# Performance work log

Hardware: AMD Instinct MI355X
Metric: run time of the kernel (lower is better)

Reference implementation:

```python
import jax, jax.numpy as jnp
import numpy as np

N, E, G = 40000, 640000, 64
D_IN, D_EMB, D_HID, D_OUT = 128, 128, 128, 36


def setup_inputs() -> dict:
    key = jax.random.key(0)
    ks = jax.random.split(key, 12)
    x = jax.random.normal(ks[0], (N, D_IN), dtype=jnp.float32)
    edge_weight = jax.random.uniform(ks[1], (E,), dtype=jnp.float32)
    rho = jax.random.uniform(ks[2], (G,), dtype=jnp.float32)
    edge_index = jax.random.randint(ks[3], (2, E), 0, N, dtype=jnp.int32)
    batch = jnp.sort(jax.random.randint(ks[4], (N,), 0, G, dtype=jnp.int32))
    def lin(k, fi, fo):
        s = 1.0 / np.sqrt(fi)
        return jax.random.normal(k, (fi, fo), dtype=jnp.float32) * s
    conv_w = lin(ks[5], D_IN, D_EMB)
    conv_b = jnp.zeros((D_EMB,), jnp.float32)
    w1 = lin(ks[6], 2 * D_EMB + 1, D_HID); b1 = jnp.zeros((D_HID,), jnp.float32)
    w2 = lin(ks[7], D_HID, D_HID);        b2 = jnp.zeros((D_HID,), jnp.float32)
    w3 = lin(ks[8], D_HID, D_OUT);        b3 = jnp.zeros((D_OUT,), jnp.float32)
    return dict(x=x, edge_weight=edge_weight, rho=rho, conv_w=conv_w, conv_b=conv_b,
                w1=w1, b1=b1, w2=w2, b2=b2, w3=w3, b3=b3,
                edge_index=edge_index, batch=batch)


def _gcn_conv(h, edge_index, ew, W, b):
    # PyG GCNConv: add self-loops (weight 1), symmetric deg^-1/2 normalization,
    # linear transform, gather-scale-scatter aggregation, bias.
    n = h.shape[0]
    loop = jnp.arange(n, dtype=edge_index.dtype)
    src = jnp.concatenate([edge_index[0], loop])
    dst = jnp.concatenate([edge_index[1], loop])
    w_all = jnp.concatenate([ew, jnp.ones((n,), ew.dtype)])
    deg = jax.ops.segment_sum(w_all, dst, num_segments=n)
    dinv = jnp.where(deg > 0, jax.lax.rsqrt(deg), 0.0)
    norm = dinv[src] * w_all * dinv[dst]          # [E+N]
    hW = h @ W                                    # [N, D_EMB]
    msg = hW[src] * norm[:, None]                 # [E+N, D_EMB]
    return jax.ops.segment_sum(msg, dst, num_segments=n) + b


def reference(x, edge_weight, rho, conv_w, conv_b, w1, b1, w2, b2, w3, b3,
              edge_index, batch):
    h = jax.nn.relu(_gcn_conv(x, edge_index, edge_weight, conv_w, conv_b))
    g = G
    cnt = jax.ops.segment_sum(jnp.ones((h.shape[0],), h.dtype), batch, num_segments=g)
    hmax = jax.ops.segment_max(h, batch, num_segments=g)
    hmax = jnp.where(cnt[:, None] > 0, hmax, 0.0)
    hsum = jax.ops.segment_sum(h, batch, num_segments=g)
    hmean = hsum / jnp.maximum(cnt, 1.0)[:, None]
    hg = jnp.concatenate([hmax, hmean, rho[:, None]], axis=1)  # [G, 2*D_EMB+1]
    z = jax.nn.relu(hg @ w1 + b1)
    z = jax.nn.relu(z @ w2 + b2)
    return z @ w3 + b3
```

## Files before the change

### kernel.cpp

```cpp
#include <hip/hip_runtime.h>
#include <hip/hip_fp16.h>

static __device__ __forceinline__ float relu_f(float v) { return v > 0.f ? v : 0.f; }

typedef _Float16 half8 __attribute__((ext_vector_type(8)));
typedef float floatx4 __attribute__((ext_vector_type(4)));

#define ELL 96

static __device__ __forceinline__ float entry_w(unsigned int pk) {
  return __half2float(__ushort_as_half((unsigned short)(pk >> 16)));
}


__global__ __launch_bounds__(256) void count_fill_kernel(
    const int* __restrict__ src, const int* __restrict__ dst,
    const float* __restrict__ ew, unsigned long long* __restrict__ cnt,
    unsigned int* __restrict__ epack, int E,
    const float* __restrict__ W, _Float16* __restrict__ wt,
    const float* __restrict__ w1, float* __restrict__ w1t,
    const float* __restrict__ w2, float* __restrict__ w2t,
    const float* __restrict__ w3, float* __restrict__ w3t) {
  int i = blockIdx.x * blockDim.x + threadIdx.x;
  if (i < 16384) {
    int k = i >> 7, c = i & 127;
    wt[c * 128 + k] = (_Float16)W[i];
  } else if (i < 16384 + 32896) {
    int j = i - 16384;
    int k = j >> 7, c = j & 127;
    w1t[c * 260 + k] = w1[j];
  } else if (i < 16384 + 32896 + 16384) {
    int j = i - (16384 + 32896);
    int k = j >> 7, c = j & 127;
    w2t[c * 128 + k] = w2[j];
  } else if (i < 16384 + 32896 + 16384 + 4608) {
    int j = i - (16384 + 32896 + 16384);
    int k = j / 36, c = j - k * 36;
    w3t[c * 128 + k] = w3[j];
  }
  int e0 = i * 4;
  if (e0 >= E) return;
  if (e0 + 3 < E) {
    int4   s4 = *(const int4*)(src + e0);
    int4   d4 = *(const int4*)(dst + e0);
    float4 w4 = *(const float4*)(ew + e0);
    int   ss[4] = {s4.x, s4.y, s4.z, s4.w};
    int   dd[4] = {d4.x, d4.y, d4.z, d4.w};
    float ww[4] = {w4.x, w4.y, w4.z, w4.w};
    #pragma unroll
    for (int u = 0; u < 4; ++u) {
      unsigned long long pk = (1ull << 32) |
          (unsigned long long)__float2uint_rn(ww[u] * 16777216.f);
      unsigned long long old = atomicAdd(&cnt[dd[u]], pk);
      unsigned int r = (unsigned int)(old >> 32);
      if (r < ELL) {
        unsigned short w16 = __half_as_ushort(__float2half_rn(ww[u]));
        epack[(size_t)dd[u] * ELL + r] = (unsigned int)ss[u] | ((unsigned int)w16 << 16);
      }
    }
  } else {
    for (int e = e0; e < E; ++e) {
      float w = ew[e];
      unsigned long long pk = (1ull << 32) |
          (unsigned long long)__float2uint_rn(w * 16777216.f);
      unsigned long long old = atomicAdd(&cnt[dst[e]], pk);
      unsigned int r = (unsigned int)(old >> 32);
      if (r < ELL) {
        unsigned short w16 = __half_as_ushort(__float2half_rn(w));
        epack[(size_t)dst[e] * ELL + r] = (unsigned int)src[e] | ((unsigned int)w16 << 16);
      }
    }
  }
}


__global__ void premul_cast_kernel(const float4* __restrict__ x4,
                                   const unsigned long long* __restrict__ cnt,
                                   half8* __restrict__ xh8, int n) {
  int j = blockIdx.x * blockDim.x + threadIdx.x;
  if (j >= n * 16) return;
  int node = j >> 4;
  unsigned long long cv = cnt[node];
  float deg = 1.f + (float)(unsigned int)cv * (1.f / 16777216.f);
  float dinv = rsqrtf(deg);
  float4 a = x4[2 * j], b = x4[2 * j + 1];
  half8 o;
  o[0] = (_Float16)(a.x * dinv); o[1] = (_Float16)(a.y * dinv);
  o[2] = (_Float16)(a.z * dinv); o[3] = (_Float16)(a.w * dinv);
  o[4] = (_Float16)(b.x * dinv); o[5] = (_Float16)(b.y * dinv);
  o[6] = (_Float16)(b.z * dinv); o[7] = (_Float16)(b.w * dinv);
  xh8[j] = o;
}


__global__ __launch_bounds__(256) void agg_gemm_pool_kernel(const half8* __restrict__ xh8,
    const unsigned long long* __restrict__ cnt,
    const unsigned int* __restrict__ epack, const _Float16* __restrict__ wt,
    const float* __restrict__ bias, const int* __restrict__ batch,
    float* __restrict__ gmax, float* __restrict__ gsum, float* __restrict__ gcnt, int n) {
  __shared__ float sH[64 * 129];
  _Float16* sAgg = (_Float16*)sH;
  __shared__ int sBatch[64];
  int tid = threadIdx.x;
  int w = tid >> 6, lane = tid & 63;
  int grp = lane >> 4, sub = lane & 15;
  int quad = lane >> 4, c15 = lane & 15;
  int row0 = blockIdx.x * 64;
  int nb = n - row0; if (nb > 64) nb = 64;

  #pragma unroll
  for (int it = 0; it < 4; ++it) {
    int rloc = w * 16 + it * 4 + grp;
    int node = row0 + rloc;
    if (node >= n) node = n - 1;
    unsigned long long cv = cnt[node];
    int deg = (int)(unsigned int)(cv >> 32);
    if (deg > ELL) deg = ELL;
    float dn = rsqrtf(1.f + (float)(unsigned int)cv * (1.f / 16777216.f));
    half8 xv = xh8[(size_t)node * 16 + sub];
    float acc[8];
    #pragma unroll
    for (int c = 0; c < 8; ++c) acc[c] = dn * (float)xv[c];
    size_t base = (size_t)node * ELL;
    int dlen = (deg + 7) & ~7;
    uint4 pa, pb;
    if (dlen > 0) {
      pa = *(const uint4*)&epack[base];
      pb = *(const uint4*)&epack[base + 4];
    }
    for (int j = 0; j < dlen; j += 8) {
      size_t nxt = (j + 8 < dlen) ? base + j + 8 : base;
      uint4 na = *(const uint4*)&epack[nxt];
      uint4 nb2 = *(const uint4*)&epack[nxt + 4];
      unsigned int pk[8] = {pa.x, pa.y, pa.z, pa.w, pb.x, pb.y, pb.z, pb.w};
      half8 hx[8];
      #pragma unroll
      for (int u = 0; u < 8; ++u) {
        int sidx = (j + u < deg) ? (int)(pk[u] & 0xFFFFu) : node;
        hx[u] = xh8[(size_t)sidx * 16 + sub];
      }
      #pragma unroll
      for (int u = 0; u < 8; ++u) {
        float wgt = (j + u < deg) ? entry_w(pk[u]) * dn : 0.f;
        #pragma unroll
        for (int c = 0; c < 8; ++c) acc[c] += wgt * (float)hx[u][c];
      }
      pa = na; pb = nb2;
    }
    half8 outv;
    #pragma unroll
    for (int c = 0; c < 8; ++c) outv[c] = (_Float16)acc[c];
    *(half8*)&sAgg[rloc * 136 + sub * 8] = outv;
  }
  __syncthreads();

  half8 af[4];
  #pragma unroll
  for (int ks = 0; ks < 4; ++ks)
    af[ks] = *(const half8*)&sAgg[(w * 16 + c15) * 136 + ks * 32 + quad * 8];
  if (tid < nb) sBatch[tid] = batch[row0 + tid];
  __syncthreads();

  float bb[8];
  #pragma unroll
  for (int j = 0; j < 8; ++j) bb[j] = bias[j * 16 + c15];

  floatx4 acc[8] = {};
  #pragma unroll
  for (int ks = 0; ks < 4; ++ks) {
    #pragma unroll
    for (int j = 0; j < 8; ++j) {
      const half8* bptr =
          (const half8*)(wt + (size_t)(j * 16 + c15) * 128 + ks * 32 + quad * 8);
      acc[j] = __builtin_amdgcn_mfma_f32_16x16x32_f16(af[ks], *bptr, acc[j], 0, 0, 0);
    }
  }

  #pragma unroll
  for (int j = 0; j < 8; ++j) {
    int col = j * 16 + c15;
    #pragma unroll
    for (int r = 0; r < 4; ++r) {
      int row = w * 16 + quad * 4 + r;
      if (row < nb) sH[row * 129 + col] = relu_f(acc[j][r] + bb[j]);
    }
  }
  __syncthreads();

  if (tid < 128) {
    int c = tid;
    int cur = sBatch[0];
    float mx = 0.f, sm = 0.f;
    int cnt_ = 0;
    for (int r = 0; r < nb; ++r) {
      int g = sBatch[r];
      if (g != cur) {
        atomicMax((int*)&gmax[cur * 128 + c], __float_as_int(mx));
        atomicAdd(&gsum[cur * 128 + c], sm);
        if (c == 0) atomicAdd(&gcnt[cur], (float)cnt_);
        mx = 0.f; sm = 0.f; cnt_ = 0; cur = g;
      }
      float v = sH[r * 129 + c];
      mx = fmaxf(mx, v);
      sm += v;
      ++cnt_;
    }
    atomicMax((int*)&gmax[cur * 128 + c], __float_as_int(mx));
    atomicAdd(&gsum[cur * 128 + c], sm);
    if (c == 0) atomicAdd(&gcnt[cur], (float)cnt_);
  }
}


__global__ __launch_bounds__(256) void mlp_kernel(const float* __restrict__ gmax,
    const float* __restrict__ gsum, const float* __restrict__ gcnt,
    const float* __restrict__ rho,
    const float* __restrict__ w1t, const float* __restrict__ b1,
    const float* __restrict__ w2t, const float* __restrict__ b2,
    const float* __restrict__ w3t, const float* __restrict__ b3,
    float* __restrict__ out) {
  __shared__ float s_in[260];
  __shared__ float s_part[256];
  __shared__ float s_z1[128];
  __shared__ float s_z2[128];
  int g = blockIdx.x, t = threadIdx.x;
  int col = t & 127, seg = t >> 7;
  float inv_cnt = 1.f / fmaxf(gcnt[g], 1.f);
  if (t < 128) s_in[t] = gmax[g * 128 + t];
  else         s_in[t] = gsum[g * 128 + col] * inv_cnt;
  if (t == 0)  s_in[256] = rho[g];
  __syncthreads();

  float s;
  {
    const float4* wp = (const float4*)(w1t + (size_t)col * 260 + seg * 128);
    const float4* sp = (const float4*)(s_in + seg * 128);
    float a = 0.f, b = 0.f;
    #pragma unroll
    for (int q = 0; q < 32; q += 2) {
      float4 u0 = wp[q],     i0 = sp[q];
      float4 u1 = wp[q + 1], i1 = sp[q + 1];
      a += u0.x * i0.x + u0.y * i0.y + u0.z * i0.z + u0.w * i0.w;
      b += u1.x * i1.x + u1.y * i1.y + u1.z * i1.z + u1.w * i1.w;
    }
    s = a + b;
    s += seg ? s_in[256] * w1t[(size_t)col * 260 + 256] : b1[col];
  }
  s_part[t] = s;
  __syncthreads();
  if (t < 128) s_z1[t] = relu_f(s_part[t] + s_part[t + 128]);
  __syncthreads();

  {
    const float4* wp = (const float4*)(w2t + (size_t)col * 128 + seg * 64);
    const float4* sp = (const float4*)(s_z1 + seg * 64);
    float a = 0.f, b = 0.f;
    #pragma unroll
    for (int q = 0; q < 16; q += 2) {
      float4 u0 = wp[q],     i0 = sp[q];
      float4 u1 = wp[q + 1], i1 = sp[q + 1];
      a += u0.x * i0.x + u0.y * i0.y + u0.z * i0.z + u0.w * i0.w;
      b += u1.x * i1.x + u1.y * i1.y + u1.z * i1.z + u1.w * i1.w;
    }
    s = a + b + (seg ? 0.f : b2[col]);
  }
  s_part[t] = s;
  __syncthreads();
  if (t < 128) s_z2[t] = relu_f(s_part[t] + s_part[t + 128]);
  __syncthreads();

  if (t < 144) {
    int oc = t % 36, sg = t / 36;
    const float4* wp = (const float4*)(w3t + (size_t)oc * 128 + sg * 32);
    const float4* sp = (const float4*)(s_z2 + sg * 32);
    float a = 0.f;
    #pragma unroll
    for (int q = 0; q < 8; ++q) {
      float4 u = wp[q], iv = sp[q];
      a += u.x * iv.x + u.y * iv.y + u.z * iv.z + u.w * iv.w;
    }
    s_part[t] = a;
  }
  __syncthreads();
  if (t < 36)
    out[g * 36 + t] = b3[t] + s_part[t] + s_part[t + 36] + s_part[t + 72] + s_part[t + 108];
}


extern "C" void kernel_launch(void* const* d_in, const int* in_sizes, int n_in,
                              void* d_out, int out_size, void* d_ws, size_t ws_size,
                              hipStream_t stream) {
  const float* x      = (const float*)d_in[0];
  const float* ew     = (const float*)d_in[1];
  const float* rho    = (const float*)d_in[2];
  const float* conv_w = (const float*)d_in[3];
  const float* conv_b = (const float*)d_in[4];
  const float* w1 = (const float*)d_in[5];
  const float* b1 = (const float*)d_in[6];
  const float* w2 = (const float*)d_in[7];
  const float* b2 = (const float*)d_in[8];
  const float* w3 = (const float*)d_in[9];
  const float* b3 = (const float*)d_in[10];
  const int* eidx  = (const int*)d_in[11];
  const int* batch = (const int*)d_in[12];

  const int N = in_sizes[0] / 128;
  const int E = in_sizes[1];
  const int G = in_sizes[2];
  const int* srcp = eidx;
  const int* dstp = eidx + E;

  char* p = (char*)d_ws;
  auto carve = [&](size_t bytes) { char* r = p; p += (bytes + 255) & ~(size_t)255; return (void*)r; };
  char* zbase = p;
  unsigned long long* cnt  = (unsigned long long*)carve((size_t)N * 8);
  float*              gmax = (float*)             carve((size_t)G * 128 * 4);
  float*              gsum = (float*)             carve((size_t)G * 128 * 4);
  float*              gcnt = (float*)             carve((size_t)G * 4);
  size_t zbytes = (size_t)(p - zbase);
  unsigned int* epack = (unsigned int*)carve((size_t)N * ELL * 4);
  half8*        xh    = (half8*)       carve((size_t)N * 128 * 2);
  _Float16*     wt    = (_Float16*)    carve((size_t)128 * 128 * 2);
  float*        w1t   = (float*)       carve((size_t)128 * 260 * 4);
  float*        w2t   = (float*)       carve((size_t)128 * 128 * 4);
  float*        w3t   = (float*)       carve((size_t)36 * 128 * 4);

  hipMemsetAsync(zbase, 0, zbytes, stream);

  int nthr_cf = (E + 3) / 4;
  if (nthr_cf < 70272) nthr_cf = 70272;
  count_fill_kernel<<<(nthr_cf + 255) / 256, 256, 0, stream>>>(srcp, dstp, ew, cnt,
                                                               epack, E, conv_w, wt,
                                                               w1, w1t, w2, w2t, w3, w3t);
  premul_cast_kernel<<<(N * 16 + 255) / 256, 256, 0, stream>>>((const float4*)x, cnt, xh, N);
  agg_gemm_pool_kernel<<<(N + 63) / 64, 256, 0, stream>>>(xh, cnt, epack, wt, conv_b,
                                                          batch, gmax, gsum, gcnt, N);
  mlp_kernel<<<G, 256, 0, stream>>>(gmax, gsum, gcnt, rho, w1t, b1, w2t, b2, w3t, b3,
                                    (float*)d_out);
}
```

Before: 173.2 us.

## Split fused aggregation+GEMM+pool kernel into separate aggregation and GEMM-pool kernels

The neighbour-gather aggregation moves out of the LDS-heavy fused kernel into its own kernel. It uses no shared memory, handles one node per 16-thread group, and writes fp16 aggregated features to a new global buffer. The GEMM/pooling kernel now reads its MFMA A-fragments straight from that buffer instead of from LDS, which drops a barrier. The aim is higher occupancy and better latency hiding for the memory-bound gather loop. The cost is an extra launch and an extra write and read of an N×128 fp16 intermediate.

```diff
diff --git a/kernel.cpp b/kernel.cpp
--- a/kernel.cpp
+++ b/kernel.cpp
@@ -93,73 +93,74 @@
 }
 
 
-__global__ __launch_bounds__(256) void agg_gemm_pool_kernel(const half8* __restrict__ xh8,
+__global__ __launch_bounds__(256) void agg_kernel(const half8* __restrict__ xh8,
     const unsigned long long* __restrict__ cnt,
-    const unsigned int* __restrict__ epack, const _Float16* __restrict__ wt,
-    const float* __restrict__ bias, const int* __restrict__ batch,
+    const unsigned int* __restrict__ epack,
+    half8* __restrict__ hagg, int n) {
+  int tid = threadIdx.x;
+  int node = blockIdx.x * 16 + (tid >> 4);
+  int sub = tid & 15;
+  if (node >= n) return;
+  unsigned long long cv = cnt[node];
+  int deg = (int)(unsigned int)(cv >> 32);
+  if (deg > ELL) deg = ELL;
+  float dn = rsqrtf(1.f + (float)(unsigned int)cv * (1.f / 16777216.f));
+  half8 xv = xh8[(size_t)node * 16 + sub];
+  float acc[8];
+  #pragma unroll
+  for (int c = 0; c < 8; ++c) acc[c] = dn * (float)xv[c];
+  size_t base = (size_t)node * ELL;
+  int dlen = (deg + 7) & ~7;
+  uint4 pa, pb;
+  if (dlen > 0) {
+    pa = *(const uint4*)&epack[base];
+    pb = *(const uint4*)&epack[base + 4];
+  }
+  for (int j = 0; j < dlen; j += 8) {
+    size_t nxt = (j + 8 < dlen) ? base + j + 8 : base;
+    uint4 na = *(const uint4*)&epack[nxt];
+    uint4 nb2 = *(const uint4*)&epack[nxt + 4];
+    unsigned int pk[8] = {pa.x, pa.y, pa.z, pa.w, pb.x, pb.y, pb.z, pb.w};
+    half8 hx[8];
+    #pragma unroll
+    for (int u = 0; u < 8; ++u) {
+      int sidx = (j + u < deg) ? (int)(pk[u] & 0xFFFFu) : node;
+      hx[u] = xh8[(size_t)sidx * 16 + sub];
+    }
+    #pragma unroll
+    for (int u = 0; u < 8; ++u) {
+      float wgt = (j + u < deg) ? entry_w(pk[u]) * dn : 0.f;
+      #pragma unroll
+      for (int c = 0; c < 8; ++c) acc[c] += wgt * (float)hx[u][c];
+    }
+    pa = na; pb = nb2;
+  }
+  half8 outv;
+  #pragma unroll
+  for (int c = 0; c < 8; ++c) outv[c] = (_Float16)acc[c];
+  hagg[(size_t)node * 16 + sub] = outv;
+}
+
+
+__global__ __launch_bounds__(256) void gemm_pool_kernel(const half8* __restrict__ hagg,
+    const _Float16* __restrict__ wt, const float* __restrict__ bias,
+    const int* __restrict__ batch,
     float* __restrict__ gmax, float* __restrict__ gsum, float* __restrict__ gcnt, int n) {
   __shared__ float sH[64 * 129];
-  _Float16* sAgg = (_Float16*)sH;
   __shared__ int sBatch[64];
   int tid = threadIdx.x;
   int w = tid >> 6, lane = tid & 63;
-  int grp = lane >> 4, sub = lane & 15;
   int quad = lane >> 4, c15 = lane & 15;
   int row0 = blockIdx.x * 64;
   int nb = n - row0; if (nb > 64) nb = 64;
 
-  #pragma unroll
-  for (int it = 0; it < 4; ++it) {
-    int rloc = w * 16 + it * 4 + grp;
-    int node = row0 + rloc;
-    if (node >= n) node = n - 1;
-    unsigned long long cv = cnt[node];
-    int deg = (int)(unsigned int)(cv >> 32);
-    if (deg > ELL) deg = ELL;
-    float dn = rsqrtf(1.f + (float)(unsigned int)cv * (1.f / 16777216.f));
-    half8 xv = xh8[(size_t)node * 16 + sub];
-    float acc[8];
-    #pragma unroll
-    for (int c = 0; c < 8; ++c) acc[c] = dn * (float)xv[c];
-    size_t base = (size_t)node * ELL;
-    int dlen = (deg + 7) & ~7;
-    uint4 pa, pb;
-    if (dlen > 0) {
-      pa = *(const uint4*)&epack[base];
-      pb = *(const uint4*)&epack[base + 4];
-    }
-    for (int j = 0; j < dlen; j += 8) {
-      size_t nxt = (j + 8 < dlen) ? base + j + 8 : base;
-      uint4 na = *(const uint4*)&epack[nxt];
-      uint4 nb2 = *(const uint4*)&epack[nxt + 4];
-      unsigned int pk[8] = {pa.x, pa.y, pa.z, pa.w, pb.x, pb.y, pb.z, pb.w};
-      half8 hx[8];
-      #pragma unroll
-      for (int u = 0; u < 8; ++u) {
-        int sidx = (j + u < deg) ? (int)(pk[u] & 0xFFFFu) : node;
-        hx[u] = xh8[(size_t)sidx * 16 + sub];
-      }
-      #pragma unroll
-      for (int u = 0; u < 8; ++u) {
-        float wgt = (j + u < deg) ? entry_w(pk[u]) * dn : 0.f;
-        #pragma unroll
-        for (int c = 0; c < 8; ++c) acc[c] += wgt * (float)hx[u][c];
-      }
-      pa = na; pb = nb2;
-    }
-    half8 outv;
-    #pragma unroll
-    for (int c = 0; c < 8; ++c) outv[c] = (_Float16)acc[c];
-    *(half8*)&sAgg[rloc * 136 + sub * 8] = outv;
-  }
-  __syncthreads();
-
+  int node = row0 + w * 16 + c15;
+  if (node >= n) node = n - 1;
   half8 af[4];
   #pragma unroll
   for (int ks = 0; ks < 4; ++ks)
-    af[ks] = *(const half8*)&sAgg[(w * 16 + c15) * 136 + ks * 32 + quad * 8];
+    af[ks] = hagg[(size_t)node * 16 + ks * 4 + quad];
   if (tid < nb) sBatch[tid] = batch[row0 + tid];
-  __syncthreads();
 
   float bb[8];
   #pragma unroll
@@ -320,6 +321,7 @@
   size_t zbytes = (size_t)(p - zbase);
   unsigned int* epack = (unsigned int*)carve((size_t)N * ELL * 4);
   half8*        xh    = (half8*)       carve((size_t)N * 128 * 2);
+  half8*        hagg  = (half8*)       carve((size_t)N * 128 * 2);
   _Float16*     wt    = (_Float16*)    carve((size_t)128 * 128 * 2);
   float*        w1t   = (float*)       carve((size_t)128 * 260 * 4);
   float*        w2t   = (float*)       carve((size_t)128 * 128 * 4);
@@ -333,8 +335,9 @@
                                                                epack, E, conv_w, wt,
                                                                w1, w1t, w2, w2t, w3, w3t);
   premul_cast_kernel<<<(N * 16 + 255) / 256, 256, 0, stream>>>((const float4*)x, cnt, xh, N);
-  agg_gemm_pool_kernel<<<(N + 63) / 64, 256, 0, stream>>>(xh, cnt, epack, wt, conv_b,
-                                                          batch, gmax, gsum, gcnt, N);
+  agg_kernel<<<(N + 15) / 16, 256, 0, stream>>>(xh, cnt, epack, hagg, N);
+  gemm_pool_kernel<<<(N + 63) / 64, 256, 0, stream>>>(hagg, wt, conv_b, batch,
+                                                      gmax, gsum, gcnt, N);
   mlp_kernel<<<G, 256, 0, stream>>>(gmax, gsum, gcnt, rho, w1t, b1, w2t, b2, w3t, b3,
                                     (float*)d_out);
 }
```

New measurement: 180.4 us. 4.2% more time.
